# Kernel optimization log

Hardware: AMD Instinct MI355X
Metric: run time of the kernel (lower is better)

## Reference

```python
import jax, jax.numpy as jnp
import numpy as np

H = 4          # heads
C = 64         # per-head channels
HID = 256      # hidden_dim = H*C
L = 4          # num_layers
N = 50000      # nodes
E = 300000     # edges
G = 64         # graphs
NODE_DIMS = [80, 16, 8]
EDGE_DIMS = [8, 4]


def setup_inputs() -> dict:
    key = jax.random.key(0)
    ks = iter(jax.random.split(key, 64))
    def nrm(shape, fan_in):
        return jax.random.normal(next(ks), shape, dtype=jnp.float32) * (1.0 / np.sqrt(fan_in))
    inp = {}
    inp['x'] = jax.random.randint(next(ks), (N, 3), 0, 8)
    inp['edge_attr'] = jax.random.randint(next(ks), (E, 2), 0, 4)
    inp['edge_index'] = jax.random.randint(next(ks), (2, E), 0, N)
    inp['batch'] = jnp.sort(jax.random.randint(next(ks), (N,), 0, G))
    inp['scalars'] = jax.random.uniform(next(ks), (G, 5), dtype=jnp.float32)
    inp['num_graphs'] = G
    # categorical embedding tables (summed per field)
    inp['node_emb0'] = nrm((NODE_DIMS[0], HID), HID)
    inp['node_emb1'] = nrm((NODE_DIMS[1], HID), HID)
    inp['node_emb2'] = nrm((NODE_DIMS[2], HID), HID)
    inp['edge_emb0'] = nrm((EDGE_DIMS[0], HID), HID)
    inp['edge_emb1'] = nrm((EDGE_DIMS[1], HID), HID)
    # stacked per-layer TransformerConv params
    inp['Wq'] = nrm((L, HID, HID), HID); inp['bq'] = jnp.zeros((L, HID))
    inp['Wk'] = nrm((L, HID, HID), HID); inp['bk'] = jnp.zeros((L, HID))
    inp['Wv'] = nrm((L, HID, HID), HID); inp['bv'] = jnp.zeros((L, HID))
    inp['We'] = nrm((L, HID, HID), HID); inp['be'] = jnp.zeros((L, HID))
    inp['Wskip'] = nrm((L, HID, HID), HID); inp['bskip'] = jnp.zeros((L, HID))
    inp['Wbeta'] = nrm((L, 3 * HID, 1), 3 * HID)  # beta gate, bias=False in PyG
    inp['ln_g'] = jnp.ones((L, HID)); inp['ln_b'] = jnp.zeros((L, HID))
    # pragma scalar encoder
    inp['pw1'] = nrm((5, HID), 5); inp['pb1'] = jnp.zeros((HID,))
    inp['pw2'] = nrm((HID, HID), HID); inp['pb2'] = jnp.zeros((HID,))
    # readout MLP
    inp['rw1'] = nrm((HID, HID), HID); inp['rb1'] = jnp.zeros((HID,))
    inp['rw2'] = nrm((HID, HID // 2), HID); inp['rb2'] = jnp.zeros((HID // 2,))
    inp['rw3'] = nrm((HID // 2, 4), HID // 2); inp['rb3'] = jnp.zeros((4,))
    return inp


def _forward(scalars, node_emb0, node_emb1, node_emb2, edge_emb0, edge_emb1,
             Wq, bq, Wk, bk, Wv, bv, We, be, Wskip, bskip, Wbeta, ln_g, ln_b,
             pw1, pb1, pw2, pb2, rw1, rb1, rw2, rb2, rw3, rb3,
             x, edge_attr, edge_index, batch, num_graphs):
    n = x.shape[0]
    src, dst = edge_index[0], edge_index[1]
    # CategoricalEmbedding: sum of per-field embeddings
    h = node_emb0[x[:, 0]] + node_emb1[x[:, 1]] + node_emb2[x[:, 2]]      # [N, HID]
    ef = edge_emb0[edge_attr[:, 0]] + edge_emb1[edge_attr[:, 1]]          # [E, HID]
    scale = 1.0 / jnp.sqrt(jnp.asarray(C, h.dtype))
    for l in range(L):
        q = (h @ Wq[l] + bq[l]).reshape(n, H, C)
        kN = (h @ Wk[l] + bk[l]).reshape(n, H, C)
        vN = (h @ Wv[l] + bv[l]).reshape(n, H, C)
        e = (ef @ We[l] + be[l]).reshape(-1, H, C)                        # [E, H, C]
        kj = kN[src] + e                                                  # edge feat added to keys
        alpha = jnp.sum(q[dst] * kj, axis=-1) * scale                     # [E, H]
        # segment softmax over incoming edges per destination node
        amax = jax.ops.segment_max(alpha, dst, num_segments=n)
        amax = jnp.where(jnp.isfinite(amax), amax, 0.0)
        ea = jnp.exp(alpha - amax[dst])
        denom = jax.ops.segment_sum(ea, dst, num_segments=n)
        attn = ea / jnp.maximum(denom, 1e-16)[dst]                        # [E, H]
        msg = (vN[src] + e) * attn[..., None]                             # edge feat added to values
        out = jax.ops.segment_sum(msg, dst, num_segments=n).reshape(n, HID)
        # beta gated skip (TransformerConv beta=True, root_weight=True)
        r = h @ Wskip[l] + bskip[l]
        beta = jax.nn.sigmoid(jnp.concatenate([out, r, out - r], axis=-1) @ Wbeta[l])  # [N,1]
        out = beta * r + (1.0 - beta) * out
        out = jax.nn.relu(out)
        # LayerNorm over hidden dim
        mu = jnp.mean(out, axis=-1, keepdims=True)
        var = jnp.var(out, axis=-1, keepdims=True)
        out = (out - mu) * jax.lax.rsqrt(var + 1e-5) * ln_g[l] + ln_b[l]
        h = h + out                                                       # residual (dropout off in eval)
    pooled = jax.ops.segment_sum(h, batch, num_segments=num_graphs)       # global_add_pool
    p = jax.nn.relu(scalars @ pw1 + pb1) @ pw2 + pb2                      # pragma encoder
    pooled = pooled + p
    z = jax.nn.relu(pooled @ rw1 + rb1)
    z = jax.nn.relu(z @ rw2 + rb2)
    return z @ rw3 + rb3                                                  # [G, 4]


def reference(x, edge_attr, edge_index, batch, scalars, num_graphs,
              node_emb0, node_emb1, node_emb2, edge_emb0, edge_emb1,
              Wq, bq, Wk, bk, Wv, bv, We, be, Wskip, bskip, Wbeta, ln_g, ln_b,
              pw1, pb1, pw2, pb2, rw1, rb1, rw2, rb2, rw3, rb3):
    return _forward(scalars, node_emb0, node_emb1, node_emb2, edge_emb0, edge_emb1,
                    Wq, bq, Wk, bk, Wv, bv, We, be, Wskip, bskip, Wbeta, ln_g, ln_b,
                    pw1, pb1, pw2, pb2, rw1, rb1, rw2, rb2, rw3, rb3,
                    x, edge_attr, edge_index, batch, num_graphs)
```

## Files before the change

kernel.cpp:

```cpp
#include <hip/hip_runtime.h>
#include <hip/hip_bf16.h>

typedef short short8 __attribute__((ext_vector_type(8)));
typedef float floatx4 __attribute__((ext_vector_type(4)));
typedef __hip_bfloat16 bf16;

#define HID 256
#define NL  4
#define AS1 __attribute__((address_space(1)))
#define AS3 __attribute__((address_space(3)))

__device__ __forceinline__ float b2f(bf16 v) { return __bfloat162float(v); }
__device__ __forceinline__ bf16 f2b(float v) { return __float2bfloat16(v); }
__device__ __forceinline__ float us2f(unsigned short u) {
    unsigned int x = ((unsigned int)u) << 16;
    return __uint_as_float(x);
}
__device__ __forceinline__ unsigned short f2us(float v) {
    bf16 t = __float2bfloat16(v);
    return *reinterpret_cast<unsigned short*>(&t);
}

template <int CTRL>
__device__ __forceinline__ float row_ror_add(float x) {
    return x + __int_as_float(__builtin_amdgcn_update_dpp(
        0, __float_as_int(x), CTRL, 0xF, 0xF, true));
}

__global__ void zero_ws_kernel(int* __restrict__ a, int* __restrict__ b, int n,
                               float* __restrict__ p, int np) {
    int i = blockIdx.x * 256 + threadIdx.x;
    if (i < n) { a[i] = 0; b[i] = 0; }
    if (i < np) p[i] = 0.f;
}

__global__ __launch_bounds__(256) void node_embed_kernel(const int* __restrict__ x,
                                  const float* __restrict__ e0, const float* __restrict__ e1,
                                  const float* __restrict__ e2,
                                  bf16* __restrict__ hbf, int N) {
    const int tid = threadIdx.x;
    const int n = blockIdx.x * 4 + (tid >> 6);
    if (n >= N) return;
    const int c4 = (tid & 63) * 4;
    const int i0 = x[n * 3], i1 = x[n * 3 + 1], i2 = x[n * 3 + 2];
    const float4 a = *reinterpret_cast<const float4*>(e0 + i0 * HID + c4);
    const float4 b = *reinterpret_cast<const float4*>(e1 + i1 * HID + c4);
    const float4 c = *reinterpret_cast<const float4*>(e2 + i2 * HID + c4);
    ushort4 o;
    o.x = f2us(a.x + b.x + c.x);
    o.y = f2us(a.y + b.y + c.y);
    o.z = f2us(a.z + b.z + c.z);
    o.w = f2us(a.w + b.w + c.w);
    *reinterpret_cast<ushort4*>(hbf + (size_t)n * HID + c4) = o;
}

__global__ void ecombo_embed_kernel(const float* __restrict__ e0, const float* __restrict__ e1,
                                    float* __restrict__ ec) {
    int i = blockIdx.x, c = threadIdx.x;
    ec[i * HID + c] = e0[(i >> 2) * HID + c] + e1[(i & 3) * HID + c];
}

__global__ void edge_prep_kernel(const int* __restrict__ ea, const int* __restrict__ dst,
                                 int E, int* __restrict__ ecid, int* __restrict__ counts) {
    int e = blockIdx.x * 256 + threadIdx.x;
    if (e < E) {
        ecid[e] = ea[e * 2] * 4 + ea[e * 2 + 1];
        atomicAdd(&counts[dst[e]], 1);
    }
}

__global__ void combo_proj_kernel(const float* __restrict__ ec, const float* __restrict__ We,
                                  const float* __restrict__ be, float* __restrict__ ecp4) {
    __shared__ float row[HID];
    int l = blockIdx.x >> 5, i = blockIdx.x & 31, c = threadIdx.x;
    row[c] = ec[i * HID + c];
    __syncthreads();
    const float* We_l = We + (size_t)l * 65536;
    float a = be[l * 256 + c];
    for (int k = 0; k < HID; ++k) a += row[k] * We_l[k * HID + c];
    ecp4[(size_t)l * 32 * HID + i * HID + c] = a;
}

__global__ void scan_local_kernel(const int* __restrict__ counts, int N,
                                  int* __restrict__ incl, int* __restrict__ bsum) {
    __shared__ int sd[256];
    int i = threadIdx.x;
    int idx = blockIdx.x * 256 + i;
    sd[i] = (idx < N) ? counts[idx] : 0;
    __syncthreads();
    for (int off = 1; off < 256; off <<= 1) {
        int t = (i >= off) ? sd[i - off] : 0;
        __syncthreads();
        sd[i] += t;
        __syncthreads();
    }
    if (idx < N) incl[idx] = sd[i];
    if (i == 255) bsum[blockIdx.x] = sd[255];
}

__global__ void scan_block_kernel(const int* __restrict__ bsum, int nb, int* __restrict__ boff) {
    __shared__ int sd[256];
    int i = threadIdx.x;
    sd[i] = (i < nb) ? bsum[i] : 0;
    __syncthreads();
    for (int off = 1; off < 256; off <<= 1) {
        int t = (i >= off) ? sd[i - off] : 0;
        __syncthreads();
        sd[i] += t;
        __syncthreads();
    }
    if (i < nb) boff[i] = (i == 0) ? 0 : sd[i - 1];
}

__global__ void scan_add_kernel(const int* __restrict__ incl, const int* __restrict__ boff,
                                int N, int* __restrict__ indptr) {
    int idx = blockIdx.x * 256 + threadIdx.x;
    if (idx < N) indptr[idx + 1] = incl[idx] + boff[blockIdx.x];
    if (idx == 0) indptr[0] = 0;
}

__global__ void fill_sorted_kernel(const int* __restrict__ dst, const int* __restrict__ srcv,
                                   const int* __restrict__ ecid, const int* __restrict__ indptr,
                                   int E, int* __restrict__ fill, int2* __restrict__ sorted2) {
    int e = blockIdx.x * 256 + threadIdx.x;
    if (e < E) {
        int d = dst[e];
        int pos = indptr[d] + atomicAdd(&fill[d], 1);
        sorted2[pos] = make_int2(srcv[e] << 11, ecid[e] << 10);
    }
    if (e < 4) sorted2[E + e] = make_int2(0, 0);
}

__global__ __launch_bounds__(256) void pack_wcat_kernel(
    const float* __restrict__ Wq, const float* __restrict__ Wk,
    const float* __restrict__ Wv, const float* __restrict__ Ws,
    bf16* __restrict__ wcatT) {
    __shared__ bf16 tile[64][65];
    const int jt = blockIdx.x;
    const int kt = blockIdx.y;
    const int l  = blockIdx.z;
    const int tid = threadIdx.x;
    const int jl = tid & 63;
    const int j = jt * 64 + jl;
    const float* W;
    int jj;
    if (j < 256)      { W = Wq; jj = j; }
    else if (j < 512) { W = Ws; jj = j - 256; }
    else {
        int g = (j - 512) >> 3, r = (j - 512) & 7;
        if (r < 4) { W = Wk; jj = 4 * g + r; }
        else       { W = Wv; jj = 4 * g + r - 4; }
    }
    const float* Wbase = W + (size_t)l * 65536 + jj + (size_t)(kt * 64) * 256;
    const int kr = tid >> 6;
#pragma unroll
    for (int i = 0; i < 16; ++i) {
        const int kl = kr + i * 4;
        tile[kl][jl] = f2b(Wbase[(size_t)kl * 256]);
    }
    __syncthreads();
    const int kl2 = tid & 63;
    const int jr = tid >> 6;
    bf16* out = wcatT + (size_t)l * 262144 + (size_t)(jt * 64) * 256 + kt * 64 + kl2;
#pragma unroll
    for (int i = 0; i < 16; ++i) {
        const int jl2 = jr + i * 4;
        out[(size_t)jl2 * 256] = tile[kl2][jl2];
    }
}

__global__ void pack_bias_kernel(const float* __restrict__ bq, const float* __restrict__ bk,
                                 const float* __restrict__ bv, const float* __restrict__ bs,
                                 float* __restrict__ bcat) {
    int idx = blockIdx.x * 256 + threadIdx.x;
    if (idx < 4096) {
        int l = idx >> 10, j = idx & 1023;
        const float* B;
        int jj;
        if (j < 256)      { B = bq; jj = j; }
        else if (j < 512) { B = bs; jj = j - 256; }
        else {
            int g = (j - 512) >> 3, r = (j - 512) & 7;
            if (r < 4) { B = bk; jj = 4 * g + r; }
            else       { B = bv; jj = 4 * g + r - 4; }
        }
        bcat[idx] = B[l * 256 + jj];
    }
}

__global__ __launch_bounds__(512) void gemm_bt_kernel(
    const bf16* __restrict__ A, const bf16* __restrict__ BT,
    const float* __restrict__ bias, bf16* __restrict__ C, int M, int Nout) {
    constexpr int BM = 128, BN = 256, BK = 64, CSTR = 136;
    __shared__ __align__(16) bf16 smem[BM * 64 + BN * 64];
    bf16* sA = smem;
    bf16* sB = smem + BM * 64;
    const int m0 = blockIdx.y * BM;
    const int n0 = blockIdx.x * BN;
    const int tid = threadIdx.x;
    const int lane = tid & 63;
    const int wave = tid >> 6;
    const int wm = (wave >> 2) * 64;
    const int wn = (wave & 3) * 64;
    const int fr = lane & 15;
    const int quad = lane >> 4;
    const int sub = lane >> 3;
    const int slot = lane & 7;
    const int jsw = slot ^ sub;
    floatx4 acc[4][4] = {};
    for (int kc = 0; kc < 256; kc += BK) {
#pragma unroll
        for (int p = 0; p < 2; ++p) {
            const int brow = (wave * 2 + p) * 8;
            const int gm = min(m0 + brow + sub, M - 1);
            __builtin_amdgcn_global_load_lds(
                (const AS1 void*)(A + (size_t)gm * 256 + kc + jsw * 8),
                (AS3 void*)(sA + brow * 64), 16, 0, 0);
        }
#pragma unroll
        for (int p = 0; p < 4; ++p) {
            const int brow = (wave * 4 + p) * 8;
            __builtin_amdgcn_global_load_lds(
                (const AS1 void*)(BT + (size_t)(n0 + brow + sub) * 256 + kc + jsw * 8),
                (AS3 void*)(sB + brow * 64), 16, 0, 0);
        }
        __syncthreads();
#pragma unroll
        for (int ks = 0; ks < BK; ks += 32) {
            const int ch = (ks >> 3) + quad;
            const int phys = (ch ^ (fr & 7)) << 3;
            short8 af[4], bfm[4];
#pragma unroll
            for (int i = 0; i < 4; ++i) {
                af[i]  = *reinterpret_cast<const short8*>(&sA[(wm + i * 16 + fr) * 64 + phys]);
                bfm[i] = *reinterpret_cast<const short8*>(&sB[(wn + i * 16 + fr) * 64 + phys]);
            }
#pragma unroll
            for (int mi = 0; mi < 4; ++mi)
#pragma unroll
                for (int ni = 0; ni < 4; ++ni)
                    acc[mi][ni] = __builtin_amdgcn_mfma_f32_16x16x32_bf16(af[mi], bfm[ni], acc[mi][ni], 0, 0, 0);
        }
        __syncthreads();
    }
    float bias4[4];
#pragma unroll
    for (int ni = 0; ni < 4; ++ni) bias4[ni] = bias[n0 + wn + ni * 16 + fr];
    bf16* sC = smem;
    const int myhalf = wn >> 7;
#pragma unroll
    for (int half = 0; half < 2; ++half) {
        if (myhalf == half) {
            const int wnl = wn & 127;
#pragma unroll
            for (int mi = 0; mi < 4; ++mi)
#pragma unroll
                for (int ni = 0; ni < 4; ++ni)
#pragma unroll
                    for (int r = 0; r < 4; ++r)
                        sC[(wm + mi * 16 + quad * 4 + r) * CSTR + wnl + ni * 16 + fr] =
                            f2b(acc[mi][ni][r] + bias4[ni]);
        }
        __syncthreads();
#pragma unroll
        for (int p = 0; p < 4; ++p) {
            int ci = tid + p * 512;
            int row = ci >> 4;
            int c8 = (ci & 15) << 3;
            if (m0 + row < M)
                *reinterpret_cast<uint4*>(C + (size_t)(m0 + row) * Nout + n0 + half * 128 + c8) =
                    *reinterpret_cast<const uint4*>(&sC[row * CSTR + c8]);
        }
        __syncthreads();
    }
}

__global__ __launch_bounds__(256) void attn_node_kernel(
    const bf16* __restrict__ qkvs,
    const float* __restrict__ ecp,
    const int* __restrict__ indptr, const int2* __restrict__ sorted2,
    const float* __restrict__ Wbeta_l, const float* __restrict__ lng, const float* __restrict__ lnb,
    bf16* __restrict__ hbf, int N) {
    const int tid = threadIdx.x;
    const int wv = tid >> 6;
    const int lane = tid & 63;
    const int n = blockIdx.x * 4 + wv;
    if (n >= N) return;
    const int c0 = lane * 4;
    const ushort4 qu = *reinterpret_cast<const ushort4*>(qkvs + (size_t)n * 1024 + c0);
    const float q0 = us2f(qu.x), q1 = us2f(qu.y), q2 = us2f(qu.z), q3 = us2f(qu.w);
    float a0 = 0.f, a1 = 0.f, a2 = 0.f, a3 = 0.f, wsum = 0.f;
    const int e0 = indptr[n], e1 = indptr[n + 1];
    const char* __restrict__ kvb = (const char*)qkvs + 1024 + lane * 16;
    const char* __restrict__ epb = (const char*)ecp + c0 * 4;

    auto edge_body = [&](const uint4& kv, const float4& ep) {
        const float k0 = us2f((unsigned short)(kv.x & 0xffff)), k1 = us2f((unsigned short)(kv.x >> 16));
        const float k2 = us2f((unsigned short)(kv.y & 0xffff)), k3 = us2f((unsigned short)(kv.y >> 16));
        const float v0 = us2f((unsigned short)(kv.z & 0xffff)), v1 = us2f((unsigned short)(kv.z >> 16));
        const float v2 = us2f((unsigned short)(kv.w & 0xffff)), v3 = us2f((unsigned short)(kv.w >> 16));
        float t = q0 * (k0 + ep.x) + q1 * (k1 + ep.y) + q2 * (k2 + ep.z) + q3 * (k3 + ep.w);
        t = row_ror_add<0x121>(t);
        t = row_ror_add<0x122>(t);
        t = row_ror_add<0x124>(t);
        t = row_ror_add<0x128>(t);
        const float w = __expf(t * 0.125f);
        a0 += w * (v0 + ep.x);
        a1 += w * (v1 + ep.y);
        a2 += w * (v2 + ep.z);
        a3 += w * (v3 + ep.w);
        wsum += w;
    };

    if (e0 < e1) {
        int2 m0 = sorted2[e0];
        int2 m1 = sorted2[e0 + 1];
        uint4 kv0 = *reinterpret_cast<const uint4*>(kvb + (unsigned)m0.x);
        uint4 kv1 = *reinterpret_cast<const uint4*>(kvb + (unsigned)m1.x);
        int ee = e0;
        for (; ee + 1 < e1; ee += 2) {
            const int2 mN0 = sorted2[ee + 2];
            const int2 mN1 = sorted2[ee + 3];
            const uint4 kvN0 = *reinterpret_cast<const uint4*>(kvb + (unsigned)mN0.x);
            const uint4 kvN1 = *reinterpret_cast<const uint4*>(kvb + (unsigned)mN1.x);
            const float4 ep0 = *reinterpret_cast<const float4*>(epb + (unsigned)m0.y);
            const float4 ep1 = *reinterpret_cast<const float4*>(epb + (unsigned)m1.y);
            edge_body(kv0, ep0);
            edge_body(kv1, ep1);
            m0 = mN0; m1 = mN1;
            kv0 = kvN0; kv1 = kvN1;
        }
        if (ee < e1) {
            const float4 ep0 = *reinterpret_cast<const float4*>(epb + (unsigned)m0.y);
            edge_body(kv0, ep0);
        }
    }
    const float inv = (wsum > 0.f) ? 1.f / wsum : 0.f;
    const float o0 = a0 * inv, o1 = a1 * inv, o2 = a2 * inv, o3 = a3 * inv;
    const ushort4 ru = *reinterpret_cast<const ushort4*>(qkvs + (size_t)n * 1024 + 256 + c0);
    const float r0 = us2f(ru.x), r1 = us2f(ru.y), r2 = us2f(ru.z), r3 = us2f(ru.w);
    const float4 w1 = *reinterpret_cast<const float4*>(Wbeta_l + c0);
    const float4 w2 = *reinterpret_cast<const float4*>(Wbeta_l + 256 + c0);
    const float4 w3 = *reinterpret_cast<const float4*>(Wbeta_l + 512 + c0);
    float tb = o0 * w1.x + o1 * w1.y + o2 * w1.z + o3 * w1.w
             + r0 * w2.x + r1 * w2.y + r2 * w2.z + r3 * w2.w
             + (o0 - r0) * w3.x + (o1 - r1) * w3.y + (o2 - r2) * w3.z + (o3 - r3) * w3.w;
#pragma unroll
    for (int off = 32; off > 0; off >>= 1) tb += __shfl_xor(tb, off);
    const float beta = 1.f / (1.f + __expf(-tb));
    float g0 = fmaxf(beta * r0 + (1.f - beta) * o0, 0.f);
    float g1 = fmaxf(beta * r1 + (1.f - beta) * o1, 0.f);
    float g2 = fmaxf(beta * r2 + (1.f - beta) * o2, 0.f);
    float g3 = fmaxf(beta * r3 + (1.f - beta) * o3, 0.f);
    float s1 = g0 + g1 + g2 + g3;
    float s2 = g0 * g0 + g1 * g1 + g2 * g2 + g3 * g3;
#pragma unroll
    for (int off = 32; off > 0; off >>= 1) { s1 += __shfl_xor(s1, off); s2 += __shfl_xor(s2, off); }
    const float mu = s1 * (1.f / 256.f);
    const float var = s2 * (1.f / 256.f) - mu * mu;
    const float rish = rsqrtf(fmaxf(var, 0.f) + 1e-5f);
    const float4 gg = *reinterpret_cast<const float4*>(lng + c0);
    const float4 bb = *reinterpret_cast<const float4*>(lnb + c0);
    ushort4 hb = *reinterpret_cast<ushort4*>(hbf + (size_t)n * HID + c0);
    float h0 = us2f(hb.x) + (g0 - mu) * rish * gg.x + bb.x;
    float h1 = us2f(hb.y) + (g1 - mu) * rish * gg.y + bb.y;
    float h2 = us2f(hb.z) + (g2 - mu) * rish * gg.z + bb.z;
    float h3 = us2f(hb.w) + (g3 - mu) * rish * gg.w + bb.w;
    hb.x = f2us(h0); hb.y = f2us(h1); hb.z = f2us(h2); hb.w = f2us(h3);
    *reinterpret_cast<ushort4*>(hbf + (size_t)n * HID + c0) = hb;
}

__global__ __launch_bounds__(256) void pool_kernel(const bf16* __restrict__ hbf,
                                                   const int* __restrict__ batch,
                                                   float* __restrict__ pooled, int N) {
    __shared__ int sb[64];
    const int c = threadIdx.x;
    const int n0 = blockIdx.x * 64;
    const int cnt = min(64, N - n0);
    if (c < 64 && c < cnt) sb[c] = batch[n0 + c];
    __syncthreads();
    float acc = 0.f;
    int gcur = sb[0];
    for (int i = 0; i < cnt; ++i) {
        const int g = sb[i];
        if (g != gcur) {
            atomicAdd(&pooled[(size_t)gcur * HID + c], acc);
            acc = 0.f;
            gcur = g;
        }
        acc += b2f(hbf[(size_t)(n0 + i) * HID + c]);
    }
    atomicAdd(&pooled[(size_t)gcur * HID + c], acc);
}

__global__ void pragma_kernel(const float* __restrict__ scalars,
                              const float* __restrict__ pw1, const float* __restrict__ pb1,
                              const float* __restrict__ pw2, const float* __restrict__ pb2,
                              float* __restrict__ pooled) {
    int g = blockIdx.x, c = threadIdx.x;
    __shared__ float s5[5];
    __shared__ float t1[256];
    if (c < 5) s5[c] = scalars[g * 5 + c];
    __syncthreads();
    float a = pb1[c];
    for (int k = 0; k < 5; ++k) a += s5[k] * pw1[k * 256 + c];
    t1[c] = fmaxf(a, 0.f);
    __syncthreads();
    float p = pb2[c];
    for (int j = 0; j < 256; ++j) p += t1[j] * pw2[j * 256 + c];
    pooled[g * 256 + c] += p;
}

__global__ void readout_kernel(const float* __restrict__ pooled,
                               const float* __restrict__ rw1, const float* __restrict__ rb1,
                               const float* __restrict__ rw2, const float* __restrict__ rb2,
                               const float* __restrict__ rw3, const float* __restrict__ rb3,
                               float* __restrict__ out) {
    int g = blockIdx.x, c = threadIdx.x;
    __shared__ float pl[256], z1[256], z2[128];
    pl[c] = pooled[g * 256 + c];
    __syncthreads();
    float z = rb1[c];
    for (int k = 0; k < 256; ++k) z += pl[k] * rw1[k * 256 + c];
    z1[c] = fmaxf(z, 0.f);
    __syncthreads();
    if (c < 128) {
        float v = rb2[c];
        for (int j = 0; j < 256; ++j) v += z1[j] * rw2[j * 128 + c];
        z2[c] = fmaxf(v, 0.f);
    }
    __syncthreads();
    if (c < 4) {
        float o = rb3[c];
        for (int j = 0; j < 128; ++j) o += z2[j] * rw3[j * 4 + c];
        out[g * 4 + c] = o;
    }
}

extern "C" void kernel_launch(void* const* d_in, const int* in_sizes, int n_in,
                              void* d_out, int out_size, void* d_ws, size_t ws_size,
                              hipStream_t stream) {
    const int* x          = (const int*)d_in[0];
    const int* edge_attr  = (const int*)d_in[1];
    const int* edge_index = (const int*)d_in[2];
    const int* batch      = (const int*)d_in[3];
    const float* scalars  = (const float*)d_in[4];
    const float* ne0 = (const float*)d_in[6];
    const float* ne1 = (const float*)d_in[7];
    const float* ne2 = (const float*)d_in[8];
    const float* ee0 = (const float*)d_in[9];
    const float* ee1 = (const float*)d_in[10];
    const float* Wq = (const float*)d_in[11];
    const float* bq = (const float*)d_in[12];
    const float* Wk = (const float*)d_in[13];
    const float* bk = (const float*)d_in[14];
    const float* Wv = (const float*)d_in[15];
    const float* bv = (const float*)d_in[16];
    const float* We = (const float*)d_in[17];
    const float* be = (const float*)d_in[18];
    const float* Wskip = (const float*)d_in[19];
    const float* bskip = (const float*)d_in[20];
    const float* Wbeta = (const float*)d_in[21];
    const float* ln_g = (const float*)d_in[22];
    const float* ln_b = (const float*)d_in[23];
    const float* pw1 = (const float*)d_in[24];
    const float* pb1 = (const float*)d_in[25];
    const float* pw2 = (const float*)d_in[26];
    const float* pb2 = (const float*)d_in[27];
    const float* rw1 = (const float*)d_in[28];
    const float* rb1 = (const float*)d_in[29];
    const float* rw2 = (const float*)d_in[30];
    const float* rb2 = (const float*)d_in[31];
    const float* rw3 = (const float*)d_in[32];
    const float* rb3 = (const float*)d_in[33];

    const int N = in_sizes[0] / 3;
    const int E = in_sizes[1] / 2;
    const int G = in_sizes[4] / 5;

    char* base = (char*)d_ws;
    size_t off = 0;
    auto carve = [&](size_t bytes) -> char* {
        char* p = base + off;
        off += (bytes + 255) & ~(size_t)255;
        return p;
    };
    bf16*  hbf    = (bf16*)carve((size_t)N * HID * 2);
    bf16*  qkvs   = (bf16*)carve((size_t)N * 1024 * 2);
    float* ec     = (float*)carve((size_t)32 * HID * 4);
    float* ecp4   = (float*)carve((size_t)NL * 32 * HID * 4);
    int*   ecid   = (int*)carve((size_t)E * 4);
    float* pooled = (float*)carve((size_t)G * HID * 4);
    bf16*  wcatT  = (bf16*)carve((size_t)NL * 1024 * 256 * 2);
    float* bcat   = (float*)carve((size_t)NL * 1024 * 4);
    int* counts   = (int*)carve((size_t)N * 4);
    int* fill     = (int*)carve((size_t)N * 4);
    int* incl     = (int*)carve((size_t)N * 4);
    int* bsum     = (int*)carve(4096);
    int* boff     = (int*)carve(4096);
    int* indptr   = (int*)carve((size_t)(N + 1) * 4);
    int2* sorted2 = (int2*)carve((size_t)(E + 4) * 8);

    const int* srcv = edge_index;
    const int* dstv = edge_index + E;

    zero_ws_kernel<<<(N + 255) / 256, 256, 0, stream>>>(counts, fill, N, pooled, G * HID);
    node_embed_kernel<<<(N + 3) / 4, 256, 0, stream>>>(x, ne0, ne1, ne2, hbf, N);
    ecombo_embed_kernel<<<32, 256, 0, stream>>>(ee0, ee1, ec);
    edge_prep_kernel<<<(E + 255) / 256, 256, 0, stream>>>(edge_attr, dstv, E, ecid, counts);
    {
        dim3 gp(16, 4, 4);
        pack_wcat_kernel<<<gp, 256, 0, stream>>>(Wq, Wk, Wv, Wskip, wcatT);
    }
    pack_bias_kernel<<<16, 256, 0, stream>>>(bq, bk, bv, bskip, bcat);
    combo_proj_kernel<<<NL * 32, 256, 0, stream>>>(ec, We, be, ecp4);

    int nsb = (N + 255) / 256;
    scan_local_kernel<<<nsb, 256, 0, stream>>>(counts, N, incl, bsum);
    scan_block_kernel<<<1, 256, 0, stream>>>(bsum, nsb, boff);
    scan_add_kernel<<<nsb, 256, 0, stream>>>(incl, boff, N, indptr);
    fill_sorted_kernel<<<(E + 255) / 256, 256, 0, stream>>>(dstv, srcv, ecid, indptr, E, fill, sorted2);

    for (int l = 0; l < NL; ++l) {
        dim3 g1(4, (N + 127) / 128);
        gemm_bt_kernel<<<g1, 512, 0, stream>>>(hbf, wcatT + (size_t)l * 1024 * 256,
                                               bcat + (size_t)l * 1024, qkvs, N, 1024);
        attn_node_kernel<<<(N + 3) / 4, 256, 0, stream>>>(qkvs, ecp4 + (size_t)l * 32 * HID,
                                                          indptr, sorted2,
                                                          Wbeta + (size_t)l * 768,
                                                          ln_g + (size_t)l * 256, ln_b + (size_t)l * 256,
                                                          hbf, N);
    }

    pool_kernel<<<(N + 63) / 64, 256, 0, stream>>>(hbf, batch, pooled, N);
    pragma_kernel<<<G, 256, 0, stream>>>(scalars, pw1, pb1, pw2, pb2, pooled);
    readout_kernel<<<G, 256, 0, stream>>>(pooled, rw1, rb1, rw2, rb2, rw3, rb3, (float*)d_out);
}
```

Measured before the change: 698.3 us.

## Replace tiled GEMM with weight-stationary persistent streaming GEMM

The QKV/skip projection GEMM now keeps a 64-column slice of the full-K weight matrix resident in LDS per block. Each block loops over 256-row strips of A, reading A fragments straight from global memory into registers, with no per-K-chunk LDS staging and no barriers in the main loop. The output is written directly from registers as scattered 2-byte stores instead of being staged through LDS for coalesced 16-byte stores. This removes the repeated weight reloads and synchronization, but risks uncoalesced A reads and output writes.

```diff
diff --git a/kernel.cpp b/kernel.cpp
--- a/kernel.cpp
+++ b/kernel.cpp
@@ -188,90 +188,71 @@
     }
 }
 
-__global__ __launch_bounds__(512) void gemm_bt_kernel(
+__global__ __launch_bounds__(256, 4) void gemm_stream_kernel(
     const bf16* __restrict__ A, const bf16* __restrict__ BT,
-    const float* __restrict__ bias, bf16* __restrict__ C, int M, int Nout) {
-    constexpr int BM = 128, BN = 256, BK = 64, CSTR = 136;
-    __shared__ __align__(16) bf16 smem[BM * 64 + BN * 64];
-    bf16* sA = smem;
-    bf16* sB = smem + BM * 64;
-    const int m0 = blockIdx.y * BM;
-    const int n0 = blockIdx.x * BN;
+    const float* __restrict__ bias, bf16* __restrict__ C, int M) {
+    __shared__ __align__(16) bf16 sW[64 * 256];
     const int tid = threadIdx.x;
     const int lane = tid & 63;
     const int wave = tid >> 6;
-    const int wm = (wave >> 2) * 64;
-    const int wn = (wave & 3) * 64;
+    const int n0 = blockIdx.x * 64;
     const int fr = lane & 15;
     const int quad = lane >> 4;
-    const int sub = lane >> 3;
-    const int slot = lane & 7;
-    const int jsw = slot ^ sub;
-    floatx4 acc[4][4] = {};
-    for (int kc = 0; kc < 256; kc += BK) {
-#pragma unroll
-        for (int p = 0; p < 2; ++p) {
-            const int brow = (wave * 2 + p) * 8;
-            const int gm = min(m0 + brow + sub, M - 1);
+    const int wsw = fr & 7;
+
+    {
+        const char* wsrc = (const char*)(BT + (size_t)n0 * 256);
+#pragma unroll
+        for (int r = 0; r < 8; ++r) {
+            const int g = r * 256 + wave * 64 + lane;
+            const int sg = g ^ ((g >> 5) & 7);
             __builtin_amdgcn_global_load_lds(
-                (const AS1 void*)(A + (size_t)gm * 256 + kc + jsw * 8),
-                (AS3 void*)(sA + brow * 64), 16, 0, 0);
-        }
-#pragma unroll
-        for (int p = 0; p < 4; ++p) {
-            const int brow = (wave * 4 + p) * 8;
-            __builtin_amdgcn_global_load_lds(
-                (const AS1 void*)(BT + (size_t)(n0 + brow + sub) * 256 + kc + jsw * 8),
-                (AS3 void*)(sB + brow * 64), 16, 0, 0);
-        }
-        __syncthreads();
-#pragma unroll
-        for (int ks = 0; ks < BK; ks += 32) {
-            const int ch = (ks >> 3) + quad;
-            const int phys = (ch ^ (fr & 7)) << 3;
-            short8 af[4], bfm[4];
-#pragma unroll
-            for (int i = 0; i < 4; ++i) {
-                af[i]  = *reinterpret_cast<const short8*>(&sA[(wm + i * 16 + fr) * 64 + phys]);
-                bfm[i] = *reinterpret_cast<const short8*>(&sB[(wn + i * 16 + fr) * 64 + phys]);
-            }
+                (const AS1 void*)(wsrc + (size_t)sg * 16),
+                (AS3 void*)(sW + (r * 256 + wave * 64) * 8), 16, 0, 0);
+        }
+    }
+    float bias4[4];
+#pragma unroll
+    for (int ni = 0; ni < 4; ++ni) bias4[ni] = bias[n0 + ni * 16 + fr];
+    __syncthreads();
+
+    for (int ms = blockIdx.y; ms * 256 < M; ms += gridDim.y) {
+        const int mrow = ms * 256 + wave * 64;
+        floatx4 acc[4][4] = {};
+        const bf16* ap[4];
+#pragma unroll
+        for (int mi = 0; mi < 4; ++mi)
+            ap[mi] = A + (size_t)min(mrow + mi * 16 + fr, M - 1) * 256 + quad * 8;
+#pragma unroll
+        for (int kk = 0; kk < 8; ++kk) {
+            const int go = (((kk << 2) | quad) ^ wsw) * 8;
+            short8 bfm[4];
+#pragma unroll
+            for (int ni = 0; ni < 4; ++ni)
+                bfm[ni] = *reinterpret_cast<const short8*>(sW + (ni * 16 + fr) * 256 + go);
+            short8 af[4];
+#pragma unroll
+            for (int mi = 0; mi < 4; ++mi)
+                af[mi] = *reinterpret_cast<const short8*>(ap[mi] + kk * 32);
 #pragma unroll
             for (int mi = 0; mi < 4; ++mi)
 #pragma unroll
                 for (int ni = 0; ni < 4; ++ni)
                     acc[mi][ni] = __builtin_amdgcn_mfma_f32_16x16x32_bf16(af[mi], bfm[ni], acc[mi][ni], 0, 0, 0);
         }
-        __syncthreads();
-    }
-    float bias4[4];
-#pragma unroll
-    for (int ni = 0; ni < 4; ++ni) bias4[ni] = bias[n0 + wn + ni * 16 + fr];
-    bf16* sC = smem;
-    const int myhalf = wn >> 7;
-#pragma unroll
-    for (int half = 0; half < 2; ++half) {
-        if (myhalf == half) {
-            const int wnl = wn & 127;
-#pragma unroll
-            for (int mi = 0; mi < 4; ++mi)
-#pragma unroll
-                for (int ni = 0; ni < 4; ++ni)
-#pragma unroll
-                    for (int r = 0; r < 4; ++r)
-                        sC[(wm + mi * 16 + quad * 4 + r) * CSTR + wnl + ni * 16 + fr] =
-                            f2b(acc[mi][ni][r] + bias4[ni]);
-        }
-        __syncthreads();
-#pragma unroll
-        for (int p = 0; p < 4; ++p) {
-            int ci = tid + p * 512;
-            int row = ci >> 4;
-            int c8 = (ci & 15) << 3;
-            if (m0 + row < M)
-                *reinterpret_cast<uint4*>(C + (size_t)(m0 + row) * Nout + n0 + half * 128 + c8) =
-                    *reinterpret_cast<const uint4*>(&sC[row * CSTR + c8]);
-        }
-        __syncthreads();
+#pragma unroll
+        for (int mi = 0; mi < 4; ++mi) {
+#pragma unroll
+            for (int r = 0; r < 4; ++r) {
+                const int row = mrow + mi * 16 + quad * 4 + r;
+                if (row < M) {
+                    bf16* crow = C + (size_t)row * 1024 + n0 + fr;
+#pragma unroll
+                    for (int ni = 0; ni < 4; ++ni)
+                        crow[ni * 16] = f2b(acc[mi][ni][r] + bias4[ni]);
+                }
+            }
+        }
     }
 }
 
@@ -522,9 +503,9 @@
     fill_sorted_kernel<<<(E + 255) / 256, 256, 0, stream>>>(dstv, srcv, ecid, indptr, E, fill, sorted2);
 
     for (int l = 0; l < NL; ++l) {
-        dim3 g1(4, (N + 127) / 128);
-        gemm_bt_kernel<<<g1, 512, 0, stream>>>(hbf, wcatT + (size_t)l * 1024 * 256,
-                                               bcat + (size_t)l * 1024, qkvs, N, 1024);
+        dim3 g1(16, 98);
+        gemm_stream_kernel<<<g1, 256, 0, stream>>>(hbf, wcatT + (size_t)l * 262144,
+                                                   bcat + (size_t)l * 1024, qkvs, N);
         attn_node_kernel<<<(N + 3) / 4, 256, 0, stream>>>(qkvs, ecp4 + (size_t)l * 32 * HID,
                                                           indptr, sorted2,
                                                           Wbeta + (size_t)l * 768,
```

Measured after the change: 1.190 ms. +70.4%, slower.
